# Kernel tuning notes

Measured on AMD Instinct MI355X. Metric: run time of the kernel, lower is better.

## Reference

```python
import jax, jax.numpy as jnp
import numpy as np
from jax.scipy.special import logsumexp

EPS = 1e-16
SINKHORN_EPS = 0.05   # entropic regularization strength
SINKHORN_ITERS = 100  # fixed iteration count (jit-friendly)
PI = np.pi


def _p3_polarrel_from_cartesian(p):
    """(px,py,pz) [B,N,3] -> (eta_rel, phi_rel, pt_rel) [B,N,3], relative to jet."""
    px, py, pz = p[..., 0], p[..., 1], p[..., 2]
    pt = jnp.sqrt(px * px + py * py + EPS)
    phi = jnp.arctan2(py + EPS, px + EPS)
    eta = jnp.arcsinh(pz / (pt + EPS))
    # jet 3-momentum: sum over particle axis (dim -2)
    jp = p.sum(axis=-2)  # [B,3]
    jpx, jpy, jpz = jp[..., 0], jp[..., 1], jp[..., 2]
    jpt = jnp.sqrt(jpx * jpx + jpy * jpy + EPS)
    jphi = jnp.arctan2(jpy + EPS, jpx + EPS)
    jeta = jnp.arcsinh(jpz / (jpt + EPS))
    eta_rel = eta - jeta[..., None]
    phi_rel = (phi - jphi[..., None] + PI) % (2.0 * PI) - PI
    pt_rel = pt / (jpt[..., None] + EPS)
    return jnp.stack([eta_rel, phi_rel, pt_rel], axis=-1)


def _sinkhorn_emd(x, y):
    """Sinkhorn-regularized EMD between particle clouds.
    x, y: [B,N,3] of (eta_rel, phi_rel, pt_rel). Returns [B]."""
    eps = SINKHORN_EPS
    # pairwise DeltaR ground cost [B,N,N]
    deta = x[..., :, None, 0] - y[..., None, :, 0]
    dphi = x[..., :, None, 1] - y[..., None, :, 1]
    C = jnp.sqrt(deta * deta + dphi * dphi + EPS)
    # pt-based marginals (pt_rel > 0 by construction), normalized
    a = x[..., 2]
    b = y[..., 2]
    a = a / (a.sum(axis=-1, keepdims=True) + EPS)
    b = b / (b.sum(axis=-1, keepdims=True) + EPS)
    log_a = jnp.log(a + EPS)
    log_b = jnp.log(b + EPS)

    f0 = jnp.zeros_like(a)
    g0 = jnp.zeros_like(b)

    def step(carry, _):
        f, g = carry
        f = eps * (log_a - logsumexp((g[:, None, :] - C) / eps, axis=-1))
        g = eps * (log_b - logsumexp((f[:, :, None] - C) / eps, axis=-2))
        return (f, g), None

    (f, g), _ = jax.lax.scan(step, (f0, g0), None, length=SINKHORN_ITERS)
    logP = (f[:, :, None] + g[:, None, :] - C) / eps  # [B,N,N] transport plan (log)
    return jnp.sum(jnp.exp(logP) * C, axis=(-2, -1))  # [B]


def setup_inputs() -> dict:
    key = jax.random.key(0)
    k1, k2 = jax.random.split(key)
    B, N = 2048, 150
    p_recons = jax.random.normal(k1, (B, N, 3), dtype=jnp.float32)
    p_target = jax.random.normal(k2, (B, N, 3), dtype=jnp.float32)
    return {"p_recons": p_recons, "p_target": p_target}


def reference(p_recons, p_target):
    x = _p3_polarrel_from_cartesian(p_recons)
    y = _p3_polarrel_from_cartesian(p_target)
    return _sinkhorn_emd(x, y).sum(0)  # scalar, matching .sum(0) over batch
```

## Files before the change

kernel.cpp:

```cpp
#include <hip/hip_runtime.h>
#include <math.h>

#define N 150
#define NP 160
#define QUART 40
#define QUADS 10
#define BLOCK 640
#define ITERS 100
#define WARM 5

#define PI_F 3.14159265358979323846f
#define TWO_PI_F 6.28318530717958647692f
#define EPS_F 1e-16f
#define EPSLN2 0.03465735902799726f
#define INV_EPSLN2 28.853900817779268f
#define NEGBIG -1e30f

#if __has_builtin(__builtin_amdgcn_exp2f)
#define FEXP2(x) __builtin_amdgcn_exp2f(x)
#else
#define FEXP2(x) exp2f(x)
#endif
#if __has_builtin(__builtin_amdgcn_logf)
#define FLOG2(x) __builtin_amdgcn_logf(x)
#else
#define FLOG2(x) log2f(x)
#endif
#if __has_builtin(__builtin_amdgcn_rcpf)
#define FRCP(x) __builtin_amdgcn_rcpf(x)
#else
#define FRCP(x) (1.0f / (x))
#endif

typedef float f2 __attribute__((ext_vector_type(2)));
union F4P { float4 v; f2 h[2]; float f[4]; };

#define KU(e) Ku[(e) >> 1][(e) & 1]
#define KT(e) Kt[(e) >> 1][(e) & 1]

__device__ __forceinline__ float blockReduceSum(float v, float* red) {
    for (int o = 32; o > 0; o >>= 1) v += __shfl_down(v, o, 64);
    const int lane = threadIdx.x & 63;
    const int wv = threadIdx.x >> 6;
    __syncthreads();
    if (lane == 0) red[wv] = v;
    __syncthreads();
    float s = 0.f;
    #pragma unroll
    for (int i = 0; i < BLOCK / 64; ++i) s += red[i];
    return s;
}

__global__ __launch_bounds__(BLOCK, 2) void emd_kernel(
    const float* __restrict__ p_recons,
    const float* __restrict__ p_target,
    float* __restrict__ out)
{
    __shared__ float xeta[N], xphi[N], yeta[N], yphi[N];
    __shared__ float l2a[N], l2b[N];
    __shared__ __align__(16) float uu[NP];
    __shared__ __align__(16) float vv[NP];
    __shared__ float red[BLOCK / 64];

    const int b = blockIdx.x;
    const int tid = threadIdx.x;

    for (int c = 0; c < 2; ++c) {
        const float* P = (c == 0 ? p_recons : p_target) + (size_t)b * (N * 3);
        float px = 0.f, py = 0.f, pz = 0.f;
        if (tid < N) {
            px = P[tid * 3 + 0];
            py = P[tid * 3 + 1];
            pz = P[tid * 3 + 2];
        }
        const float jx = blockReduceSum(px, red);
        const float jy = blockReduceSum(py, red);
        const float jz = blockReduceSum(pz, red);
        const float jpt  = sqrtf(jx * jx + jy * jy + EPS_F);
        const float jphi = atan2f(jy + EPS_F, jx + EPS_F);
        const float jeta = asinhf(jz / (jpt + EPS_F));

        float ptrel = 0.f, erel = 0.f, prel = 0.f;
        if (tid < N) {
            const float pt  = sqrtf(px * px + py * py + EPS_F);
            const float phi = atan2f(py + EPS_F, px + EPS_F);
            const float eta = asinhf(pz / (pt + EPS_F));
            erel = eta - jeta;
            float d = phi - jphi + PI_F;
            d = fmodf(d, TWO_PI_F);
            if (d < 0.f) d += TWO_PI_F;
            prel = d - PI_F;
            ptrel = pt / (jpt + EPS_F);
        }
        const float spt = blockReduceSum(ptrel, red);
        if (tid < N) {
            const float aa = ptrel / (spt + EPS_F);
            if (c == 0) { xeta[tid] = erel; xphi[tid] = prel; l2a[tid] = FLOG2(aa + EPS_F); }
            else        { yeta[tid] = erel; yphi[tid] = prel; l2b[tid] = FLOG2(aa + EPS_F); }
        }
    }
    __syncthreads();

    const int r = (tid >> 2) < N ? (tid >> 2) : (N - 1);
    const int q = tid & 3;
    const bool writer = (q == 0) && ((tid >> 2) < N);
    const bool act = (tid >> 2) < N;

    f2 Ku[QUART / 2];
    f2 Kt[QUART / 2];
    {
        const float xe = xeta[r], xp = xphi[r];
        const float ye = yeta[r], yp = yphi[r];
        #pragma unroll
        for (int s = 0; s < QUART; ++s) {
            const int j = q * QUART + s;
            float ku = NEGBIG, kt = NEGBIG;
            if (j < N) {
                float de = xe - yeta[j], dp = xp - yphi[j];
                ku = -sqrtf(de * de + dp * dp + EPS_F) * INV_EPSLN2;
                de = xeta[j] - ye; dp = xphi[j] - yp;
                kt = -sqrtf(de * de + dp * dp + EPS_F) * INV_EPSLN2;
            }
            KU(s) = ku;
            KT(s) = kt;
        }
    }
    if (tid < NP) {
        const float z = (tid < N) ? 0.f : NEGBIG;
        uu[tid] = z; vv[tid] = z;
    }
    __syncthreads();

    for (int it = 0; it < WARM; ++it) {
        {
            const float4* vp = (const float4*)&vv[q * QUART];
            float mx = -3e38f;
            #pragma unroll
            for (int s = 0; s < QUADS; ++s) {
                F4P v4; v4.v = vp[s];
                mx = fmaxf(mx, fmaxf(fmaxf(v4.f[0] + KU(4*s),   v4.f[1] + KU(4*s+1)),
                                     fmaxf(v4.f[2] + KU(4*s+2), v4.f[3] + KU(4*s+3))));
            }
            mx = fmaxf(mx, __shfl_xor(mx, 1, 64));
            mx = fmaxf(mx, __shfl_xor(mx, 2, 64));
            float s0 = 0.f, s1 = 0.f, s2 = 0.f, s3 = 0.f;
            #pragma unroll
            for (int s = 0; s < QUADS; ++s) {
                F4P v4; v4.v = vp[s];
                s0 += FEXP2(v4.f[0] + KU(4*s)   - mx);
                s1 += FEXP2(v4.f[1] + KU(4*s+1) - mx);
                s2 += FEXP2(v4.f[2] + KU(4*s+2) - mx);
                s3 += FEXP2(v4.f[3] + KU(4*s+3) - mx);
            }
            float ss = (s0 + s1) + (s2 + s3);
            ss += __shfl_xor(ss, 1, 64);
            ss += __shfl_xor(ss, 2, 64);
            if (writer) uu[r] = l2a[r] - (mx + FLOG2(fmaxf(ss, 1e-37f)));
        }
        __syncthreads();
        {
            const float4* up = (const float4*)&uu[q * QUART];
            float mx = -3e38f;
            #pragma unroll
            for (int s = 0; s < QUADS; ++s) {
                F4P u4; u4.v = up[s];
                mx = fmaxf(mx, fmaxf(fmaxf(u4.f[0] + KT(4*s),   u4.f[1] + KT(4*s+1)),
                                     fmaxf(u4.f[2] + KT(4*s+2), u4.f[3] + KT(4*s+3))));
            }
            mx = fmaxf(mx, __shfl_xor(mx, 1, 64));
            mx = fmaxf(mx, __shfl_xor(mx, 2, 64));
            float s0 = 0.f, s1 = 0.f, s2 = 0.f, s3 = 0.f;
            #pragma unroll
            for (int s = 0; s < QUADS; ++s) {
                F4P u4; u4.v = up[s];
                s0 += FEXP2(u4.f[0] + KT(4*s)   - mx);
                s1 += FEXP2(u4.f[1] + KT(4*s+1) - mx);
                s2 += FEXP2(u4.f[2] + KT(4*s+2) - mx);
                s3 += FEXP2(u4.f[3] + KT(4*s+3) - mx);
            }
            float ss = (s0 + s1) + (s2 + s3);
            ss += __shfl_xor(ss, 1, 64);
            ss += __shfl_xor(ss, 2, 64);
            if (writer) vv[r] = l2b[r] - (mx + FLOG2(fmaxf(ss, 1e-37f)));
        }
        __syncthreads();
    }

    float am, bm, fin, Vh6;
    {
        const float4* vp = (const float4*)&vv[q * QUART];
        float mx = -3e38f;
        #pragma unroll
        for (int s = 0; s < QUADS; ++s) {
            F4P v4; v4.v = vp[s];
            mx = fmaxf(mx, fmaxf(fmaxf(v4.f[0] + KU(4*s),   v4.f[1] + KU(4*s+1)),
                                 fmaxf(v4.f[2] + KU(4*s+2), v4.f[3] + KU(4*s+3))));
        }
        mx = fmaxf(mx, __shfl_xor(mx, 1, 64));
        mx = fmaxf(mx, __shfl_xor(mx, 2, 64));
        float s0 = 0.f, s1 = 0.f, s2 = 0.f, s3 = 0.f;
        #pragma unroll
        for (int s = 0; s < QUADS; ++s) {
            F4P v4; v4.v = vp[s];
            KU(4*s)   = FEXP2(v4.f[0] + KU(4*s)   - mx);
            KU(4*s+1) = FEXP2(v4.f[1] + KU(4*s+1) - mx);
            KU(4*s+2) = FEXP2(v4.f[2] + KU(4*s+2) - mx);
            KU(4*s+3) = FEXP2(v4.f[3] + KU(4*s+3) - mx);
            s0 += KU(4*s); s1 += KU(4*s+1); s2 += KU(4*s+2); s3 += KU(4*s+3);
        }
        float ss = (s0 + s1) + (s2 + s3);
        ss += __shfl_xor(ss, 1, 64);
        ss += __shfl_xor(ss, 2, 64);
        am  = ss;
        fin = FEXP2(l2a[r]) * FRCP(ss);
        if (writer) uu[r] = l2a[r] - (mx + FLOG2(ss));
    }
    __syncthreads();
    {
        const float4* up = (const float4*)&uu[q * QUART];
        float mx = -3e38f;
        #pragma unroll
        for (int s = 0; s < QUADS; ++s) {
            F4P u4; u4.v = up[s];
            mx = fmaxf(mx, fmaxf(fmaxf(u4.f[0] + KT(4*s),   u4.f[1] + KT(4*s+1)),
                                 fmaxf(u4.f[2] + KT(4*s+2), u4.f[3] + KT(4*s+3))));
        }
        mx = fmaxf(mx, __shfl_xor(mx, 1, 64));
        mx = fmaxf(mx, __shfl_xor(mx, 2, 64));
        float s0 = 0.f, s1 = 0.f, s2 = 0.f, s3 = 0.f;
        #pragma unroll
        for (int s = 0; s < QUADS; ++s) {
            F4P u4; u4.v = up[s];
            KT(4*s)   = FEXP2(u4.f[0] + KT(4*s)   - mx);
            KT(4*s+1) = FEXP2(u4.f[1] + KT(4*s+1) - mx);
            KT(4*s+2) = FEXP2(u4.f[2] + KT(4*s+2) - mx);
            KT(4*s+3) = FEXP2(u4.f[3] + KT(4*s+3) - mx);
            s0 += KT(4*s); s1 += KT(4*s+1); s2 += KT(4*s+2); s3 += KT(4*s+3);
        }
        float ssv = (s0 + s1) + (s2 + s3);
        ssv += __shfl_xor(ssv, 1, 64);
        ssv += __shfl_xor(ssv, 2, 64);
        const float v5r = vv[r];
        float t = l2b[r] - (mx + FLOG2(ssv)) - v5r;
        t = fminf(t, 100.f);
        Vh6 = FEXP2(t);
        bm  = Vh6 * ssv;
    }
    __syncthreads();
    if (writer) { uu[r] = 1.0f; vv[r] = Vh6; }
    if (tid >= N && tid < NP) { uu[tid] = 0.f; vv[tid] = 0.f; }
    __syncthreads();

    for (int it = WARM + 1; it < ITERS; ++it) {
        {
            const float4* vp = (const float4*)&vv[q * QUART];
            f2 a0 = {0.f, 0.f}, a1 = {0.f, 0.f};
            #pragma unroll
            for (int s = 0; s < QUADS; ++s) {
                F4P v4; v4.v = vp[s];
                a0 += v4.h[0] * Ku[2*s];
                a1 += v4.h[1] * Ku[2*s+1];
            }
            float ss = (a0[0] + a1[0]) + (a0[1] + a1[1]);
            ss += __shfl_xor(ss, 1, 64);
            ss += __shfl_xor(ss, 2, 64);
            if (writer) uu[r] = fminf(am * FRCP(fmaxf(ss, 1e-30f)), 1e30f);
        }
        __syncthreads();
        {
            const float4* up = (const float4*)&uu[q * QUART];
            f2 a0 = {0.f, 0.f}, a1 = {0.f, 0.f};
            #pragma unroll
            for (int s = 0; s < QUADS; ++s) {
                F4P u4; u4.v = up[s];
                a0 += u4.h[0] * Kt[2*s];
                a1 += u4.h[1] * Kt[2*s+1];
            }
            float ss = (a0[0] + a1[0]) + (a0[1] + a1[1]);
            ss += __shfl_xor(ss, 1, 64);
            ss += __shfl_xor(ss, 2, 64);
            if (writer) vv[r] = fminf(bm * FRCP(fmaxf(ss, 1e-30f)), 1e30f);
        }
        __syncthreads();
        if (((it - WARM - 1) & 7) == 7) {
            const float4* vp = (const float4*)&vv[q * QUART];
            float M = 0.f;
            #pragma unroll
            for (int s = 0; s < QUADS; ++s) {
                F4P v4; v4.v = vp[s];
                Ku[2*s]   *= v4.h[0];
                Ku[2*s+1] *= v4.h[1];
                M = fmaxf(M, fmaxf(fmaxf(Ku[2*s][0], Ku[2*s][1]),
                                   fmaxf(Ku[2*s+1][0], Ku[2*s+1][1])));
            }
            M = fmaxf(M, __shfl_xor(M, 1, 64));
            M = fmaxf(M, __shfl_xor(M, 2, 64));
            M = fmaxf(M, 1e-30f);
            const float rM = FRCP(M);
            const f2 rM2 = {rM, rM};
            #pragma unroll
            for (int i = 0; i < QUART / 2; ++i) Ku[i] *= rM2;

            const float4* up = (const float4*)&uu[q * QUART];
            float Mv = 0.f;
            #pragma unroll
            for (int s = 0; s < QUADS; ++s) {
                F4P u4; u4.v = up[s];
                Kt[2*s]   *= u4.h[0];
                Kt[2*s+1] *= u4.h[1];
                Mv = fmaxf(Mv, fmaxf(fmaxf(Kt[2*s][0], Kt[2*s][1]),
                                     fmaxf(Kt[2*s+1][0], Kt[2*s+1][1])));
            }
            Mv = fmaxf(Mv, __shfl_xor(Mv, 1, 64));
            Mv = fmaxf(Mv, __shfl_xor(Mv, 2, 64));
            Mv = fmaxf(Mv, 1e-30f);
            const float rMv = FRCP(Mv);
            const f2 rMv2 = {rMv, rMv};
            #pragma unroll
            for (int i = 0; i < QUART / 2; ++i) Kt[i] *= rMv2;

            const float Uh = uu[r], Vh = vv[r];
            am  = fminf(am * rM  * FRCP(fmaxf(Uh, 1e-30f)), 1e30f);
            bm  = fminf(bm * rMv * FRCP(fmaxf(Vh, 1e-30f)), 1e30f);
            fin = fminf(fin * M * Uh, 1e30f);
            __syncthreads();
            if (writer) { uu[r] = 1.0f; vv[r] = 1.0f; }
            __syncthreads();
        }
    }

    float acc = 0.f;
    if (act) {
        const float u2 = fin * uu[r];
        const float xe = xeta[r], xp = xphi[r];
        const float4* vp = (const float4*)&vv[q * QUART];
        #pragma unroll
        for (int s = 0; s < QUADS; ++s) {
            F4P v4; v4.v = vp[s];
            #pragma unroll
            for (int k = 0; k < 4; ++k) {
                const int j = q * QUART + 4 * s + k;
                if (j < N) {
                    const float de = xe - yeta[j];
                    const float dp = xp - yphi[j];
                    const float C = sqrtf(de * de + dp * dp + EPS_F);
                    acc += u2 * v4.f[k] * KU(4 * s + k) * C;
                }
            }
        }
    }
    if (!act) acc = 0.f;
    acc = blockReduceSum(acc, red);
    if (tid == 0) atomicAdd(out, acc);
}

extern "C" void kernel_launch(void* const* d_in, const int* in_sizes, int n_in,
                              void* d_out, int out_size, void* d_ws, size_t ws_size,
                              hipStream_t stream) {
    const float* pr = (const float*)d_in[0];
    const float* pt = (const float*)d_in[1];
    float* out = (float*)d_out;
    const int B = in_sizes[0] / (N * 3);
    hipMemsetAsync(d_out, 0, sizeof(float) * out_size, stream);
    hipLaunchKernelGGL(emd_kernel, dim3(B), dim3(BLOCK), 0, stream, pr, pt, out);
}
```

Measured before the change: 948.3 us.

## Use DPP quad reductions, packed max, fused jet reduction, rarer rescaling

Replaces the __shfl_xor quad reductions with DPP quad_perm row operations, which avoid LDS-routed bpermute traffic. Computes the warm-up max with packed two-wide max, and merges the three jet-momentum block reductions into one pass with fewer barriers. It also halves how often the scaled kernels are rebased (every 16 iterations instead of 8). That saves barriers and work but raises the risk of overflow or underflow in the scaling-domain iterations.

```diff
diff --git a/kernel.cpp b/kernel.cpp
--- a/kernel.cpp
+++ b/kernel.cpp
@@ -35,8 +35,32 @@
 typedef float f2 __attribute__((ext_vector_type(2)));
 union F4P { float4 v; f2 h[2]; float f[4]; };
 
+#if __has_builtin(__builtin_elementwise_max)
+#define F2MAX(a, b) __builtin_elementwise_max((a), (b))
+#else
+__device__ __forceinline__ f2 f2max_fb(f2 a, f2 b) {
+    f2 r; r[0] = fmaxf(a[0], b[0]); r[1] = fmaxf(a[1], b[1]); return r;
+}
+#define F2MAX(a, b) f2max_fb((a), (b))
+#endif
+
 #define KU(e) Ku[(e) >> 1][(e) & 1]
 #define KT(e) Kt[(e) >> 1][(e) & 1]
+
+__device__ __forceinline__ float dpp_xor1(float x) {
+    return __int_as_float(__builtin_amdgcn_update_dpp(
+        0, __float_as_int(x), 0xB1, 0xF, 0xF, true));
+}
+__device__ __forceinline__ float dpp_xor2(float x) {
+    return __int_as_float(__builtin_amdgcn_update_dpp(
+        0, __float_as_int(x), 0x4E, 0xF, 0xF, true));
+}
+__device__ __forceinline__ float quad_sum(float x) {
+    x += dpp_xor1(x); x += dpp_xor2(x); return x;
+}
+__device__ __forceinline__ float quad_max(float x) {
+    x = fmaxf(x, dpp_xor1(x)); x = fmaxf(x, dpp_xor2(x)); return x;
+}
 
 __device__ __forceinline__ float blockReduceSum(float v, float* red) {
     for (int o = 32; o > 0; o >>= 1) v += __shfl_down(v, o, 64);
@@ -49,6 +73,27 @@
     #pragma unroll
     for (int i = 0; i < BLOCK / 64; ++i) s += red[i];
     return s;
+}
+
+__device__ __forceinline__ void blockReduceSum3(
+    float& x, float& y, float& z, float* red)
+{
+    for (int o = 32; o > 0; o >>= 1) {
+        x += __shfl_down(x, o, 64);
+        y += __shfl_down(y, o, 64);
+        z += __shfl_down(z, o, 64);
+    }
+    const int lane = threadIdx.x & 63;
+    const int wv = threadIdx.x >> 6;
+    __syncthreads();
+    if (lane == 0) { red[wv] = x; red[wv + 16] = y; red[wv + 32] = z; }
+    __syncthreads();
+    float sx = 0.f, sy = 0.f, sz = 0.f;
+    #pragma unroll
+    for (int i = 0; i < BLOCK / 64; ++i) {
+        sx += red[i]; sy += red[i + 16]; sz += red[i + 32];
+    }
+    x = sx; y = sy; z = sz;
 }
 
 __global__ __launch_bounds__(BLOCK, 2) void emd_kernel(
@@ -60,7 +105,7 @@
     __shared__ float l2a[N], l2b[N];
     __shared__ __align__(16) float uu[NP];
     __shared__ __align__(16) float vv[NP];
-    __shared__ float red[BLOCK / 64];
+    __shared__ float red[48];
 
     const int b = blockIdx.x;
     const int tid = threadIdx.x;
@@ -73,9 +118,8 @@
             py = P[tid * 3 + 1];
             pz = P[tid * 3 + 2];
         }
-        const float jx = blockReduceSum(px, red);
-        const float jy = blockReduceSum(py, red);
-        const float jz = blockReduceSum(pz, red);
+        float jx = px, jy = py, jz = pz;
+        blockReduceSum3(jx, jy, jz, red);
         const float jpt  = sqrtf(jx * jx + jy * jy + EPS_F);
         const float jphi = atan2f(jy + EPS_F, jx + EPS_F);
         const float jeta = asinhf(jz / (jpt + EPS_F));
@@ -134,15 +178,14 @@
     for (int it = 0; it < WARM; ++it) {
         {
             const float4* vp = (const float4*)&vv[q * QUART];
-            float mx = -3e38f;
+            f2 m2 = {-3e38f, -3e38f};
             #pragma unroll
             for (int s = 0; s < QUADS; ++s) {
                 F4P v4; v4.v = vp[s];
-                mx = fmaxf(mx, fmaxf(fmaxf(v4.f[0] + KU(4*s),   v4.f[1] + KU(4*s+1)),
-                                     fmaxf(v4.f[2] + KU(4*s+2), v4.f[3] + KU(4*s+3))));
-            }
-            mx = fmaxf(mx, __shfl_xor(mx, 1, 64));
-            mx = fmaxf(mx, __shfl_xor(mx, 2, 64));
+                m2 = F2MAX(m2, v4.h[0] + Ku[2*s]);
+                m2 = F2MAX(m2, v4.h[1] + Ku[2*s+1]);
+            }
+            float mx = quad_max(fmaxf(m2[0], m2[1]));
             float s0 = 0.f, s1 = 0.f, s2 = 0.f, s3 = 0.f;
             #pragma unroll
             for (int s = 0; s < QUADS; ++s) {
@@ -152,23 +195,20 @@
                 s2 += FEXP2(v4.f[2] + KU(4*s+2) - mx);
                 s3 += FEXP2(v4.f[3] + KU(4*s+3) - mx);
             }
-            float ss = (s0 + s1) + (s2 + s3);
-            ss += __shfl_xor(ss, 1, 64);
-            ss += __shfl_xor(ss, 2, 64);
+            float ss = quad_sum((s0 + s1) + (s2 + s3));
             if (writer) uu[r] = l2a[r] - (mx + FLOG2(fmaxf(ss, 1e-37f)));
         }
         __syncthreads();
         {
             const float4* up = (const float4*)&uu[q * QUART];
-            float mx = -3e38f;
+            f2 m2 = {-3e38f, -3e38f};
             #pragma unroll
             for (int s = 0; s < QUADS; ++s) {
                 F4P u4; u4.v = up[s];
-                mx = fmaxf(mx, fmaxf(fmaxf(u4.f[0] + KT(4*s),   u4.f[1] + KT(4*s+1)),
-                                     fmaxf(u4.f[2] + KT(4*s+2), u4.f[3] + KT(4*s+3))));
-            }
-            mx = fmaxf(mx, __shfl_xor(mx, 1, 64));
-            mx = fmaxf(mx, __shfl_xor(mx, 2, 64));
+                m2 = F2MAX(m2, u4.h[0] + Kt[2*s]);
+                m2 = F2MAX(m2, u4.h[1] + Kt[2*s+1]);
+            }
+            float mx = quad_max(fmaxf(m2[0], m2[1]));
             float s0 = 0.f, s1 = 0.f, s2 = 0.f, s3 = 0.f;
             #pragma unroll
             for (int s = 0; s < QUADS; ++s) {
@@ -178,9 +218,7 @@
                 s2 += FEXP2(u4.f[2] + KT(4*s+2) - mx);
                 s3 += FEXP2(u4.f[3] + KT(4*s+3) - mx);
             }
-            float ss = (s0 + s1) + (s2 + s3);
-            ss += __shfl_xor(ss, 1, 64);
-            ss += __shfl_xor(ss, 2, 64);
+            float ss = quad_sum((s0 + s1) + (s2 + s3));
             if (writer) vv[r] = l2b[r] - (mx + FLOG2(fmaxf(ss, 1e-37f)));
         }
         __syncthreads();
@@ -189,15 +227,14 @@
     float am, bm, fin, Vh6;
     {
         const float4* vp = (const float4*)&vv[q * QUART];
-        float mx = -3e38f;
+        f2 m2 = {-3e38f, -3e38f};
         #pragma unroll
         for (int s = 0; s < QUADS; ++s) {
             F4P v4; v4.v = vp[s];
-            mx = fmaxf(mx, fmaxf(fmaxf(v4.f[0] + KU(4*s),   v4.f[1] + KU(4*s+1)),
-                                 fmaxf(v4.f[2] + KU(4*s+2), v4.f[3] + KU(4*s+3))));
-        }
-        mx = fmaxf(mx, __shfl_xor(mx, 1, 64));
-        mx = fmaxf(mx, __shfl_xor(mx, 2, 64));
+            m2 = F2MAX(m2, v4.h[0] + Ku[2*s]);
+            m2 = F2MAX(m2, v4.h[1] + Ku[2*s+1]);
+        }
+        float mx = quad_max(fmaxf(m2[0], m2[1]));
         float s0 = 0.f, s1 = 0.f, s2 = 0.f, s3 = 0.f;
         #pragma unroll
         for (int s = 0; s < QUADS; ++s) {
@@ -208,9 +245,7 @@
             KU(4*s+3) = FEXP2(v4.f[3] + KU(4*s+3) - mx);
             s0 += KU(4*s); s1 += KU(4*s+1); s2 += KU(4*s+2); s3 += KU(4*s+3);
         }
-        float ss = (s0 + s1) + (s2 + s3);
-        ss += __shfl_xor(ss, 1, 64);
-        ss += __shfl_xor(ss, 2, 64);
+        float ss = quad_sum((s0 + s1) + (s2 + s3));
         am  = ss;
         fin = FEXP2(l2a[r]) * FRCP(ss);
         if (writer) uu[r] = l2a[r] - (mx + FLOG2(ss));
@@ -218,15 +253,14 @@
     __syncthreads();
     {
         const float4* up = (const float4*)&uu[q * QUART];
-        float mx = -3e38f;
+        f2 m2 = {-3e38f, -3e38f};
         #pragma unroll
         for (int s = 0; s < QUADS; ++s) {
             F4P u4; u4.v = up[s];
-            mx = fmaxf(mx, fmaxf(fmaxf(u4.f[0] + KT(4*s),   u4.f[1] + KT(4*s+1)),
-                                 fmaxf(u4.f[2] + KT(4*s+2), u4.f[3] + KT(4*s+3))));
-        }
-        mx = fmaxf(mx, __shfl_xor(mx, 1, 64));
-        mx = fmaxf(mx, __shfl_xor(mx, 2, 64));
+            m2 = F2MAX(m2, u4.h[0] + Kt[2*s]);
+            m2 = F2MAX(m2, u4.h[1] + Kt[2*s+1]);
+        }
+        float mx = quad_max(fmaxf(m2[0], m2[1]));
         float s0 = 0.f, s1 = 0.f, s2 = 0.f, s3 = 0.f;
         #pragma unroll
         for (int s = 0; s < QUADS; ++s) {
@@ -237,9 +271,7 @@
             KT(4*s+3) = FEXP2(u4.f[3] + KT(4*s+3) - mx);
             s0 += KT(4*s); s1 += KT(4*s+1); s2 += KT(4*s+2); s3 += KT(4*s+3);
         }
-        float ssv = (s0 + s1) + (s2 + s3);
-        ssv += __shfl_xor(ssv, 1, 64);
-        ssv += __shfl_xor(ssv, 2, 64);
+        float ssv = quad_sum((s0 + s1) + (s2 + s3));
         const float v5r = vv[r];
         float t = l2b[r] - (mx + FLOG2(ssv)) - v5r;
         t = fminf(t, 100.f);
@@ -261,9 +293,7 @@
                 a0 += v4.h[0] * Ku[2*s];
                 a1 += v4.h[1] * Ku[2*s+1];
             }
-            float ss = (a0[0] + a1[0]) + (a0[1] + a1[1]);
-            ss += __shfl_xor(ss, 1, 64);
-            ss += __shfl_xor(ss, 2, 64);
+            float ss = quad_sum((a0[0] + a1[0]) + (a0[1] + a1[1]));
             if (writer) uu[r] = fminf(am * FRCP(fmaxf(ss, 1e-30f)), 1e30f);
         }
         __syncthreads();
@@ -276,13 +306,11 @@
                 a0 += u4.h[0] * Kt[2*s];
                 a1 += u4.h[1] * Kt[2*s+1];
             }
-            float ss = (a0[0] + a1[0]) + (a0[1] + a1[1]);
-            ss += __shfl_xor(ss, 1, 64);
-            ss += __shfl_xor(ss, 2, 64);
+            float ss = quad_sum((a0[0] + a1[0]) + (a0[1] + a1[1]));
             if (writer) vv[r] = fminf(bm * FRCP(fmaxf(ss, 1e-30f)), 1e30f);
         }
         __syncthreads();
-        if (((it - WARM - 1) & 7) == 7) {
+        if (((it - WARM - 1) & 15) == 15) {
             const float4* vp = (const float4*)&vv[q * QUART];
             float M = 0.f;
             #pragma unroll
@@ -293,8 +321,7 @@
                 M = fmaxf(M, fmaxf(fmaxf(Ku[2*s][0], Ku[2*s][1]),
                                    fmaxf(Ku[2*s+1][0], Ku[2*s+1][1])));
             }
-            M = fmaxf(M, __shfl_xor(M, 1, 64));
-            M = fmaxf(M, __shfl_xor(M, 2, 64));
+            M = quad_max(M);
             M = fmaxf(M, 1e-30f);
             const float rM = FRCP(M);
             const f2 rM2 = {rM, rM};
@@ -311,8 +338,7 @@
                 Mv = fmaxf(Mv, fmaxf(fmaxf(Kt[2*s][0], Kt[2*s][1]),
                                      fmaxf(Kt[2*s+1][0], Kt[2*s+1][1])));
             }
-            Mv = fmaxf(Mv, __shfl_xor(Mv, 1, 64));
-            Mv = fmaxf(Mv, __shfl_xor(Mv, 2, 64));
+            Mv = quad_max(Mv);
             Mv = fmaxf(Mv, 1e-30f);
             const float rMv = FRCP(Mv);
             const f2 rMv2 = {rMv, rMv};
```

Result: faster. 867.9 us (-8.5%).
